# Performance work log

Measured on AMD Instinct MI355X. Metric: run time of the kernel, lower is better.

The kernel has to match this reference:

```python
import jax, jax.numpy as jnp
import numpy as np

B, S, V, E, H = 4096, 64, 100000, 128, 128

_PARAM_NAMES = ["Wz", "Uzl", "Uzr", "Wr", "Url", "Urr", "Wh", "Uhl", "Uhr"]


def setup_inputs() -> dict:
    key = jax.random.key(0)
    ks = jax.random.split(key, 2 + 2 * len(_PARAM_NAMES))
    inp = {"tokens": jax.random.randint(ks[0], (B, S), 0, V)}
    inp["emb"] = jax.random.normal(ks[1], (V, E), jnp.float32)
    i = 2
    for n in _PARAM_NAMES:
        din = E if n.startswith("W") else H
        inp[n] = jax.random.normal(ks[i], (din, H), jnp.float32) / np.sqrt(din).astype(np.float32)
        i += 1
        inp["b" + n] = jax.random.normal(ks[i], (H,), jnp.float32) * 0.01
        i += 1
    return inp


def _tree_gru(word, hl, hr, p):
    # word: [..., E], hl/hr: [..., H]
    z = jax.nn.sigmoid(word @ p["Wz"] + p["bWz"] + hl @ p["Uzl"] + p["bUzl"] + hr @ p["Uzr"] + p["bUzr"])
    r = jax.nn.sigmoid(word @ p["Wr"] + p["bWr"] + hl @ p["Url"] + p["bUrl"] + hr @ p["Urr"] + p["bUrr"])
    h_tilde = jnp.tanh(word @ p["Wh"] + p["bWh"] + (r * hl) @ p["Uhl"] + p["bUhl"] + (r * hr) @ p["Uhr"] + p["bUhr"])
    return z * hl + z * hr + (1.0 - z) * h_tilde


def reference(tokens, emb, Wz, bWz, Uzl, bUzl, Uzr, bUzr, Wr, bWr, Url, bUrl, Urr, bUrr, Wh, bWh, Uhl, bUhl, Uhr, bUhr):
    p = dict(Wz=Wz, bWz=bWz, Uzl=Uzl, bUzl=bUzl, Uzr=Uzr, bUzr=bUzr,
             Wr=Wr, bWr=bWr, Url=Url, bUrl=bUrl, Urr=Urr, bUrr=bUrr,
             Wh=Wh, bWh=bWh, Uhl=Uhl, bUhl=bUhl, Uhr=Uhr, bUhr=bUhr)
    x = emb[tokens]                                   # [B, S, E]
    h0 = jnp.zeros(x.shape[:2] + (H,), x.dtype)
    cur = _tree_gru(x, h0, h0, p)                     # leaf nodes [B, S, H]
    n = cur.shape[1]
    while n > 1:                                      # static loop over log2(S) tree levels
        left, right = cur[:, 0::2], cur[:, 1::2]      # pair adjacent nodes
        word0 = jnp.zeros(left.shape[:2] + (E,), cur.dtype)
        cur = _tree_gru(word0, left, right, p)
        n //= 2
    return cur.transpose(1, 0, 2)                     # [1, B, H] (matches torch transpose(0,1))
```

## Files before the change

kernel.cpp:

```cpp
#include <hip/hip_runtime.h>


typedef _Float16 half_t;
typedef __attribute__((ext_vector_type(8))) _Float16 f16x8;
typedef __attribute__((ext_vector_type(4))) float f32x4;

#define NTOK 262144
#define NB 4096
#define NV 100000

__device__ __forceinline__ float sigm(float x){
  float e = __expf(-x);
  return __builtin_amdgcn_rcpf(1.0f + e);
}
__device__ __forceinline__ float tanh_(float x){
  float xc = fminf(fmaxf(x,-15.f),15.f);
  float e = __expf(2.f*xc);
  return (e - 1.f) * __builtin_amdgcn_rcpf(e + 1.f);
}

__global__ void bias_k(const float* bWz,const float* bUzl,const float* bUzr,
                       const float* bWr,const float* bUrl,const float* bUrr,
                       const float* bWh,const float* bUhl,const float* bUhr, float* bc){
  int j = threadIdx.x;
  if (j < 128)      bc[j] = bWz[j]+bUzl[j]+bUzr[j];
  else if (j < 256){ int i=j-128; bc[j] = bWr[i]+bUrl[i]+bUrr[i]; }
  else if (j < 384){ int i=j-256; bc[j] = bWh[i]+bUhl[i]+bUhr[i]; }
}

__global__ __launch_bounds__(256) void wprep_k(
    const float* Wz, const float* Wh,
    const float* Uzl,const float* Uzr,const float* Url,const float* Urr,
    const float* Uhl,const float* Uhr, half_t* wb){
  int idx = blockIdx.x*256 + threadIdx.x;
  if (idx < 32768){
    const float* W = (idx < 16384) ? Wz : Wh;
    int t = idx & 16383;
    int w = t >> 11, ks = (t >> 9) & 3, l = (t >> 3) & 63, j = t & 7;
    int n = w*16 + (l & 15);
    int k = ks*32 + ((l >> 4) << 3) + j;
    wb[idx] = (half_t)W[k*128 + n];
  } else {
    int t = idx - 32768;
    int mat = t >> 15;
    t &= 32767;
    int w = t >> 12, ks = (t >> 9) & 7, l = (t >> 3) & 63, j = t & 7;
    int n = w*16 + (l & 15);
    int kp = ks*32 + ((l >> 4) << 3) + j;
    int k = kp >> 1;
    const float* U;
    if (mat == 0) U = (kp & 1) ? Uzr : Uzl;
    else if (mat == 1) U = (kp & 1) ? Urr : Url;
    else U = (kp & 1) ? Uhr : Uhl;
    wb[idx] = (half_t)U[k*128 + n];
  }
}

template<int MT>
__global__ __launch_bounds__(512, 4) void h1tab_k(
    const float* __restrict__ emb,
    const half_t* __restrict__ Wz_f, const half_t* __restrict__ Wh_f,
    const float* __restrict__ bc, half_t* __restrict__ t1)
{
  __shared__ __align__(16) _Float16 xs[MT*16][136];
  const int tid = threadIdx.x;
  const int m0  = blockIdx.x*(MT*16);
  #pragma unroll
  for (int it = 0; it < MT; it++){
    int idx = it*512 + tid;
    int m = idx >> 5, c = idx & 31;
    int row = m0 + m; if (row >= NV) row = 0;
    float4 v = ((const float4*)(emb + (size_t)row*128))[c];
    union { half_t h[4]; ushort4 u; } p;
    p.h[0]=(half_t)v.x; p.h[1]=(half_t)v.y; p.h[2]=(half_t)v.z; p.h[3]=(half_t)v.w;
    *(ushort4*)&xs[m][c*4] = p.u;
  }
  __syncthreads();
  const int w = tid>>6, l = tid&63;
  const int lr = l&15, lk = (l>>4)*8, lq = (l>>4)*4;
  const int col = w*16 + lr;

  f32x4 zacc[MT] = {}; f32x4 hacc[MT] = {};
  const half_t* wzp = Wz_f + ((w*4)*64 + l)*8;
  const half_t* whp = Wh_f + ((w*4)*64 + l)*8;
  f16x8 bz_n = *(const f16x8*)wzp;
  f16x8 bh_n = *(const f16x8*)whp;
  #pragma unroll
  for (int ks=0; ks<4; ks++){
    f16x8 bz = bz_n, bh = bh_n;
    if (ks < 3){
      bz_n = *(const f16x8*)(wzp + (ks+1)*512);
      bh_n = *(const f16x8*)(whp + (ks+1)*512);
    }
    #pragma unroll
    for (int mt=0; mt<MT; mt++){
      f16x8 a = *(const f16x8*)&xs[mt*16 + lr][ks*32 + lk];
      zacc[mt] = __builtin_amdgcn_mfma_f32_16x16x32_f16(a, bz, zacc[mt],0,0,0);
      hacc[mt] = __builtin_amdgcn_mfma_f32_16x16x32_f16(a, bh, hacc[mt],0,0,0);
    }
  }
  const float bzv = bc[col], bhv = bc[256+col];
  #pragma unroll
  for (int mt=0; mt<MT; mt++){
    #pragma unroll
    for (int q=0; q<4; q++){
      int row = m0 + mt*16 + lq + q;
      if (row < NV){
        float z  = sigm(zacc[mt][q] + bzv);
        float ht = tanh_(hacc[mt][q] + bhv);
        t1[(size_t)row*128 + col] = (half_t)((1.f-z)*ht);
      }
    }
  }
}

template<int MT, int GATHER>
__global__ __launch_bounds__(512, 4) void tree_k(
    const half_t* __restrict__ hin, const int* __restrict__ tokens,
    half_t* __restrict__ hout, float* __restrict__ outf,
    const half_t* __restrict__ Uz_f, const half_t* __restrict__ Ur_f, const half_t* __restrict__ Uh_f,
    const float* __restrict__ bc, int last)
{
  __shared__ __align__(16) _Float16 xs[MT*16][264];
  const int tid = threadIdx.x;
  const int m0  = blockIdx.x*(MT*16);
  #pragma unroll
  for (int it = 0; it < MT; it++){
    int idx = it*512 + tid;
    int m = idx >> 5, c = idx & 31;
    const half_t *pl, *pr;
    if (GATHER){
      int tl = tokens[2*(m0+m)], tr = tokens[2*(m0+m)+1];
      pl = hin + (size_t)tl*128 + c*4;
      pr = hin + (size_t)tr*128 + c*4;
    } else {
      size_t base = (size_t)(2*(m0+m))*128 + c*4;
      pl = hin + base;
      pr = hin + base + 128;
    }
    uint2 A  = *(const uint2*)pl;
    uint2 Bv = *(const uint2*)pr;
    uint4 o;
    o.x = (A.x & 0xFFFFu) | (Bv.x << 16);
    o.y = (A.x >> 16)     | (Bv.x & 0xFFFF0000u);
    o.z = (A.y & 0xFFFFu) | (Bv.y << 16);
    o.w = (A.y >> 16)     | (Bv.y & 0xFFFF0000u);
    *(uint4*)&xs[m][c*8] = o;
  }
  __syncthreads();
  const int w = tid>>6, l = tid&63;
  const int lr = l&15, lk = (l>>4)*8, lq = (l>>4)*4;
  const int col = w*16 + lr;

  f32x4 zacc[MT] = {}; f32x4 racc[MT] = {};
  const half_t* uzp = Uz_f + ((w*8)*64 + l)*8;
  const half_t* urp = Ur_f + ((w*8)*64 + l)*8;
  f16x8 bz_n = *(const f16x8*)uzp;
  f16x8 br_n = *(const f16x8*)urp;
  #pragma unroll
  for (int ks=0; ks<8; ks++){
    f16x8 bz = bz_n, br = br_n;
    if (ks < 7){
      bz_n = *(const f16x8*)(uzp + (ks+1)*512);
      br_n = *(const f16x8*)(urp + (ks+1)*512);
    }
    #pragma unroll
    for (int mt=0; mt<MT; mt++){
      f16x8 a = *(const f16x8*)&xs[mt*16 + lr][ks*32 + lk];
      zacc[mt] = __builtin_amdgcn_mfma_f32_16x16x32_f16(a, bz, zacc[mt],0,0,0);
      racc[mt] = __builtin_amdgcn_mfma_f32_16x16x32_f16(a, br, racc[mt],0,0,0);
    }
  }
  __syncthreads();

  uint zp[MT][2], sp[MT][2];
  const float bzv = bc[col], brv = bc[128+col];
  #pragma unroll
  for (int mt=0; mt<MT; mt++){
    union { half_t h[4]; uint u[2]; } pz, ps;
    #pragma unroll
    for (int q=0; q<4; q++){
      int row = mt*16 + lq + q;
      union { uint u; half_t h[2]; } io;
      io.u = *(uint*)&xs[row][2*col];
      float hl = (float)io.h[0];
      float hr = (float)io.h[1];
      float z  = sigm(zacc[mt][q] + bzv);
      float rv = sigm(racc[mt][q] + brv);
      pz.h[q] = (half_t)z;
      ps.h[q] = (half_t)(hl + hr);
      io.h[0] = (half_t)(rv*hl);
      io.h[1] = (half_t)(rv*hr);
      *(uint*)&xs[row][2*col] = io.u;
    }
    zp[mt][0]=pz.u[0]; zp[mt][1]=pz.u[1];
    sp[mt][0]=ps.u[0]; sp[mt][1]=ps.u[1];
  }
  __syncthreads();

  f32x4 ha[MT] = {};
  const half_t* uhp = Uh_f + ((w*8)*64 + l)*8;
  f16x8 bh_n = *(const f16x8*)uhp;
  #pragma unroll
  for (int ks=0; ks<8; ks++){
    f16x8 bh = bh_n;
    if (ks < 7) bh_n = *(const f16x8*)(uhp + (ks+1)*512);
    #pragma unroll
    for (int mt=0; mt<MT; mt++){
      f16x8 a = *(const f16x8*)&xs[mt*16 + lr][ks*32 + lk];
      ha[mt] = __builtin_amdgcn_mfma_f32_16x16x32_f16(a, bh, ha[mt],0,0,0);
    }
  }
  const float bhv = bc[256+col];
  #pragma unroll
  for (int mt=0; mt<MT; mt++){
    union { half_t h[4]; uint u[2]; } pz, ps;
    pz.u[0]=zp[mt][0]; pz.u[1]=zp[mt][1];
    ps.u[0]=sp[mt][0]; ps.u[1]=sp[mt][1];
    #pragma unroll
    for (int q=0; q<4; q++){
      int row = mt*16 + lq + q;
      float ht = tanh_(ha[mt][q] + bhv);
      float z  = (float)pz.h[q];
      float o  = z*(float)ps.h[q] + (1.f-z)*ht;
      size_t off = (size_t)(m0+row)*128 + col;
      if (last) outf[off] = o;
      else      hout[off] = (half_t)o;
    }
  }
}

extern "C" void kernel_launch(void* const* d_in, const int* in_sizes, int n_in,
                              void* d_out, int out_size, void* d_ws, size_t ws_size,
                              hipStream_t stream) {
  const int*   tokens = (const int*)  d_in[0];
  const float* emb    = (const float*)d_in[1];
  const float* Wz  = (const float*)d_in[2];  const float* bWz  = (const float*)d_in[3];
  const float* Uzl = (const float*)d_in[4];  const float* bUzl = (const float*)d_in[5];
  const float* Uzr = (const float*)d_in[6];  const float* bUzr = (const float*)d_in[7];
  const float* Wr  = (const float*)d_in[8];  const float* bWr  = (const float*)d_in[9];
  const float* Url = (const float*)d_in[10]; const float* bUrl = (const float*)d_in[11];
  const float* Urr = (const float*)d_in[12]; const float* bUrr = (const float*)d_in[13];
  const float* Wh  = (const float*)d_in[14]; const float* bWh  = (const float*)d_in[15];
  const float* Uhl = (const float*)d_in[16]; const float* bUhl = (const float*)d_in[17];
  const float* Uhr = (const float*)d_in[18]; const float* bUhr = (const float*)d_in[19];

  float*  bc = (float*)d_ws;
  half_t* wb = (half_t*)((char*)d_ws + 4096);
  half_t* Wz_f = wb;
  half_t* Wh_f = wb + 16384;
  half_t* Uz_f = wb + 32768;
  half_t* Ur_f = wb + 65536;
  half_t* Uh_f = wb + 98304;
  half_t* t1 = (half_t*)((char*)d_ws + (1<<20));
  half_t* hA = t1 + (size_t)NV*128;
  half_t* hB = hA + (size_t)(NTOK/2)*128;

  bias_k<<<1, 384, 0, stream>>>(bWz,bUzl,bUzr,bWr,bUrl,bUrr,bWh,bUhl,bUhr, bc);
  wprep_k<<<512, 256, 0, stream>>>(Wz,Wh,Uzl,Uzr,Url,Urr,Uhl,Uhr, wb);

  h1tab_k<8><<<(NV + 127)/128, 512, 0, stream>>>(emb, Wz_f, Wh_f, bc, t1);

  tree_k<8,1><<<(NTOK/2)/128, 512, 0, stream>>>(t1, tokens, hA, (float*)d_out,
                                                Uz_f, Ur_f, Uh_f, bc, 0);
  const half_t* src = hA;
  half_t* other = hB;
  for (int lvl = 2; lvl <= 6; lvl++){
    int M = NB << (6 - lvl);
    int last = (lvl == 6);
    half_t* dst = other;
    if (M >= 32768){
      tree_k<8,0><<<M/128, 512, 0, stream>>>(src, tokens, dst, (float*)d_out,
                                             Uz_f, Ur_f, Uh_f, bc, last);
    } else if (M >= 16384){
      tree_k<4,0><<<M/64, 512, 0, stream>>>(src, tokens, dst, (float*)d_out,
                                            Uz_f, Ur_f, Uh_f, bc, last);
    } else {
      tree_k<2,0><<<M/32, 512, 0, stream>>>(src, tokens, dst, (float*)d_out,
                                            Uz_f, Ur_f, Uh_f, bc, last);
    }
    other = (half_t*)src;
    src = dst;
  }
}
```

Measured before the change: 149.8 us.

## Switch tree GRU kernel to 32x32x16 MFMA with row-group wave tiling

Replaces the 16x16x32 MFMA tiles in the tree kernel with 32x32x16 MFMA, reorganising waves into column groups and row groups, and re-packs the U weight fragments to match. Launch shapes per level are rewritten: larger row tiles for early levels and smaller blocks for the final levels. The intent is to cut per-wave instruction and LDS-read overhead and to reuse each weight fragment across more rows. In exchange the accumulators grow (16 floats per tile), which raises register pressure, and the deepest levels run only 128 blocks.

```diff
diff --git a/kernel.cpp b/kernel.cpp
--- a/kernel.cpp
+++ b/kernel.cpp
@@ -4,6 +4,7 @@
 typedef _Float16 half_t;
 typedef __attribute__((ext_vector_type(8))) _Float16 f16x8;
 typedef __attribute__((ext_vector_type(4))) float f32x4;
+typedef __attribute__((ext_vector_type(16))) float f32x16;
 
 #define NTOK 262144
 #define NB 4096
@@ -44,9 +45,9 @@
     int t = idx - 32768;
     int mat = t >> 15;
     t &= 32767;
-    int w = t >> 12, ks = (t >> 9) & 7, l = (t >> 3) & 63, j = t & 7;
-    int n = w*16 + (l & 15);
-    int kp = ks*32 + ((l >> 4) << 3) + j;
+    int cg = t >> 13, ks = (t >> 9) & 15, l = (t >> 3) & 63, j = t & 7;
+    int n = cg*32 + (l & 31);
+    int kp = ks*16 + ((l >> 5) << 3) + j;
     int k = kp >> 1;
     const float* U;
     if (mat == 0) U = (kp & 1) ? Uzr : Uzl;
@@ -114,19 +115,21 @@
   }
 }
 
-template<int MT, int GATHER>
-__global__ __launch_bounds__(512, 4) void tree_k(
+template<int MT, int WR, int GATHER>
+__global__ __launch_bounds__(WR*256, 4) void tree_k(
     const half_t* __restrict__ hin, const int* __restrict__ tokens,
     half_t* __restrict__ hout, float* __restrict__ outf,
     const half_t* __restrict__ Uz_f, const half_t* __restrict__ Ur_f, const half_t* __restrict__ Uh_f,
     const float* __restrict__ bc, int last)
 {
-  __shared__ __align__(16) _Float16 xs[MT*16][264];
+  constexpr int ROWS = WR*MT*32;
+  constexpr int THREADS = WR*256;
+  __shared__ __align__(16) _Float16 xs[ROWS][264];
   const int tid = threadIdx.x;
-  const int m0  = blockIdx.x*(MT*16);
-  #pragma unroll
-  for (int it = 0; it < MT; it++){
-    int idx = it*512 + tid;
+  const int m0  = blockIdx.x*ROWS;
+  #pragma unroll
+  for (int it = 0; it < MT*4; it++){
+    int idx = it*THREADS + tid;
     int m = idx >> 5, c = idx & 31;
     const half_t *pl, *pr;
     if (GATHER){
@@ -149,80 +152,83 @@
   }
   __syncthreads();
   const int w = tid>>6, l = tid&63;
-  const int lr = l&15, lk = (l>>4)*8, lq = (l>>4)*4;
-  const int col = w*16 + lr;
-
-  f32x4 zacc[MT] = {}; f32x4 racc[MT] = {};
-  const half_t* uzp = Uz_f + ((w*8)*64 + l)*8;
-  const half_t* urp = Ur_f + ((w*8)*64 + l)*8;
+  const int cg = w & 3, rg = w >> 2;
+  const int lc = l & 31, hi = l >> 5;
+  const int lk8 = hi*8;
+  const int col = cg*32 + lc;
+  const int rowbase = rg*(MT*32);
+
+  f32x16 zacc[MT] = {}; f32x16 racc[MT] = {};
+  const half_t* uzp = Uz_f + ((cg*16)*64 + l)*8;
+  const half_t* urp = Ur_f + ((cg*16)*64 + l)*8;
   f16x8 bz_n = *(const f16x8*)uzp;
   f16x8 br_n = *(const f16x8*)urp;
   #pragma unroll
-  for (int ks=0; ks<8; ks++){
+  for (int ks=0; ks<16; ks++){
     f16x8 bz = bz_n, br = br_n;
-    if (ks < 7){
+    if (ks < 15){
       bz_n = *(const f16x8*)(uzp + (ks+1)*512);
       br_n = *(const f16x8*)(urp + (ks+1)*512);
     }
     #pragma unroll
     for (int mt=0; mt<MT; mt++){
-      f16x8 a = *(const f16x8*)&xs[mt*16 + lr][ks*32 + lk];
-      zacc[mt] = __builtin_amdgcn_mfma_f32_16x16x32_f16(a, bz, zacc[mt],0,0,0);
-      racc[mt] = __builtin_amdgcn_mfma_f32_16x16x32_f16(a, br, racc[mt],0,0,0);
-    }
-  }
-  __syncthreads();
-
-  uint zp[MT][2], sp[MT][2];
+      f16x8 a = *(const f16x8*)&xs[rowbase + mt*32 + lc][ks*16 + lk8];
+      zacc[mt] = __builtin_amdgcn_mfma_f32_32x32x16_f16(a, bz, zacc[mt],0,0,0);
+      racc[mt] = __builtin_amdgcn_mfma_f32_32x32x16_f16(a, br, racc[mt],0,0,0);
+    }
+  }
+  __syncthreads();
+
+  uint zp[MT][8], sp[MT][8];
   const float bzv = bc[col], brv = bc[128+col];
   #pragma unroll
   for (int mt=0; mt<MT; mt++){
-    union { half_t h[4]; uint u[2]; } pz, ps;
-    #pragma unroll
-    for (int q=0; q<4; q++){
-      int row = mt*16 + lq + q;
+    union { half_t h[16]; uint u[8]; } pz, ps;
+    #pragma unroll
+    for (int r=0; r<16; r++){
+      int row = rowbase + mt*32 + (r&3) + 8*(r>>2) + 4*hi;
       union { uint u; half_t h[2]; } io;
       io.u = *(uint*)&xs[row][2*col];
       float hl = (float)io.h[0];
       float hr = (float)io.h[1];
-      float z  = sigm(zacc[mt][q] + bzv);
-      float rv = sigm(racc[mt][q] + brv);
-      pz.h[q] = (half_t)z;
-      ps.h[q] = (half_t)(hl + hr);
+      float z  = sigm(zacc[mt][r] + bzv);
+      float rv = sigm(racc[mt][r] + brv);
+      pz.h[r] = (half_t)z;
+      ps.h[r] = (half_t)(hl + hr);
       io.h[0] = (half_t)(rv*hl);
       io.h[1] = (half_t)(rv*hr);
       *(uint*)&xs[row][2*col] = io.u;
     }
-    zp[mt][0]=pz.u[0]; zp[mt][1]=pz.u[1];
-    sp[mt][0]=ps.u[0]; sp[mt][1]=ps.u[1];
-  }
-  __syncthreads();
-
-  f32x4 ha[MT] = {};
-  const half_t* uhp = Uh_f + ((w*8)*64 + l)*8;
+    #pragma unroll
+    for (int u8=0; u8<8; u8++){ zp[mt][u8]=pz.u[u8]; sp[mt][u8]=ps.u[u8]; }
+  }
+  __syncthreads();
+
+  f32x16 ha[MT] = {};
+  const half_t* uhp = Uh_f + ((cg*16)*64 + l)*8;
   f16x8 bh_n = *(const f16x8*)uhp;
   #pragma unroll
-  for (int ks=0; ks<8; ks++){
+  for (int ks=0; ks<16; ks++){
     f16x8 bh = bh_n;
-    if (ks < 7) bh_n = *(const f16x8*)(uhp + (ks+1)*512);
+    if (ks < 15) bh_n = *(const f16x8*)(uhp + (ks+1)*512);
     #pragma unroll
     for (int mt=0; mt<MT; mt++){
-      f16x8 a = *(const f16x8*)&xs[mt*16 + lr][ks*32 + lk];
-      ha[mt] = __builtin_amdgcn_mfma_f32_16x16x32_f16(a, bh, ha[mt],0,0,0);
+      f16x8 a = *(const f16x8*)&xs[rowbase + mt*32 + lc][ks*16 + lk8];
+      ha[mt] = __builtin_amdgcn_mfma_f32_32x32x16_f16(a, bh, ha[mt],0,0,0);
     }
   }
   const float bhv = bc[256+col];
   #pragma unroll
   for (int mt=0; mt<MT; mt++){
-    union { half_t h[4]; uint u[2]; } pz, ps;
-    pz.u[0]=zp[mt][0]; pz.u[1]=zp[mt][1];
-    ps.u[0]=sp[mt][0]; ps.u[1]=sp[mt][1];
-    #pragma unroll
-    for (int q=0; q<4; q++){
-      int row = mt*16 + lq + q;
-      float ht = tanh_(ha[mt][q] + bhv);
-      float z  = (float)pz.h[q];
-      float o  = z*(float)ps.h[q] + (1.f-z)*ht;
+    union { half_t h[16]; uint u[8]; } pz, ps;
+    #pragma unroll
+    for (int u8=0; u8<8; u8++){ pz.u[u8]=zp[mt][u8]; ps.u[u8]=sp[mt][u8]; }
+    #pragma unroll
+    for (int r=0; r<16; r++){
+      int row = rowbase + mt*32 + (r&3) + 8*(r>>2) + 4*hi;
+      float ht = tanh_(ha[mt][r] + bhv);
+      float z  = (float)pz.h[r];
+      float o  = z*(float)ps.h[r] + (1.f-z)*ht;
       size_t off = (size_t)(m0+row)*128 + col;
       if (last) outf[off] = o;
       else      hout[off] = (half_t)o;
@@ -261,25 +267,11 @@
 
   h1tab_k<8><<<(NV + 127)/128, 512, 0, stream>>>(emb, Wz_f, Wh_f, bc, t1);
 
-  tree_k<8,1><<<(NTOK/2)/128, 512, 0, stream>>>(t1, tokens, hA, (float*)d_out,
-                                                Uz_f, Ur_f, Uh_f, bc, 0);
-  const half_t* src = hA;
-  half_t* other = hB;
-  for (int lvl = 2; lvl <= 6; lvl++){
-    int M = NB << (6 - lvl);
-    int last = (lvl == 6);
-    half_t* dst = other;
-    if (M >= 32768){
-      tree_k<8,0><<<M/128, 512, 0, stream>>>(src, tokens, dst, (float*)d_out,
-                                             Uz_f, Ur_f, Uh_f, bc, last);
-    } else if (M >= 16384){
-      tree_k<4,0><<<M/64, 512, 0, stream>>>(src, tokens, dst, (float*)d_out,
-                                            Uz_f, Ur_f, Uh_f, bc, last);
-    } else {
-      tree_k<2,0><<<M/32, 512, 0, stream>>>(src, tokens, dst, (float*)d_out,
-                                            Uz_f, Ur_f, Uh_f, bc, last);
-    }
-    other = (half_t*)src;
-    src = dst;
-  }
-}
+  float* outf = (float*)d_out;
+  tree_k<2,2,1><<<1024, 512, 0, stream>>>(t1, tokens, hA, outf, Uz_f, Ur_f, Uh_f, bc, 0);
+  tree_k<2,2,0><<<512, 512, 0, stream>>>(hA, tokens, hB, outf, Uz_f, Ur_f, Uh_f, bc, 0);
+  tree_k<2,2,0><<<256, 512, 0, stream>>>(hB, tokens, hA, outf, Uz_f, Ur_f, Uh_f, bc, 0);
+  tree_k<2,2,0><<<128, 512, 0, stream>>>(hA, tokens, hB, outf, Uz_f, Ur_f, Uh_f, bc, 0);
+  tree_k<1,2,0><<<128, 512, 0, stream>>>(hB, tokens, hA, outf, Uz_f, Ur_f, Uh_f, bc, 0);
+  tree_k<1,1,0><<<128, 256, 0, stream>>>(hA, tokens, hB, outf, Uz_f, Ur_f, Uh_f, bc, 1);
+}
```

Result: slower. 156.7 us (+4.6%).

## Fuse tree levels two through six into one shared-memory kernel

Applied to the files above, without the earlier changes.

Replaces the five per-level tree kernel launches with a single tail kernel. Each block loads 128 level-1 nodes and runs the remaining levels in LDS, passing intermediate states between two shared buffers, so the intermediate global writes and reads are gone. Bias folding moves into the weight-prep kernel, the tanh formulation is simplified, and h1tab uses smaller tiles with higher occupancy. The cost is that later levels run on small, partly empty tiles, with extra syncs and idle MFMA work.

```diff
diff --git a/kernel.cpp b/kernel.cpp
--- a/kernel.cpp
+++ b/kernel.cpp
@@ -2,6 +2,7 @@
 
 
 typedef _Float16 half_t;
+typedef __attribute__((ext_vector_type(2))) _Float16 f16x2;
 typedef __attribute__((ext_vector_type(8))) _Float16 f16x8;
 typedef __attribute__((ext_vector_type(4))) float f32x4;
 
@@ -14,24 +15,19 @@
   return __builtin_amdgcn_rcpf(1.0f + e);
 }
 __device__ __forceinline__ float tanh_(float x){
-  float xc = fminf(fmaxf(x,-15.f),15.f);
-  float e = __expf(2.f*xc);
-  return (e - 1.f) * __builtin_amdgcn_rcpf(e + 1.f);
-}
-
-__global__ void bias_k(const float* bWz,const float* bUzl,const float* bUzr,
-                       const float* bWr,const float* bUrl,const float* bUrr,
-                       const float* bWh,const float* bUhl,const float* bUhr, float* bc){
-  int j = threadIdx.x;
-  if (j < 128)      bc[j] = bWz[j]+bUzl[j]+bUzr[j];
-  else if (j < 256){ int i=j-128; bc[j] = bWr[i]+bUrl[i]+bUrr[i]; }
-  else if (j < 384){ int i=j-256; bc[j] = bWh[i]+bUhl[i]+bUhr[i]; }
+  float e = __expf(2.f*x);
+  float r = __builtin_amdgcn_rcpf(1.0f + e);
+  return __builtin_fmaf(-2.0f, r, 1.0f);
 }
 
 __global__ __launch_bounds__(256) void wprep_k(
     const float* Wz, const float* Wh,
     const float* Uzl,const float* Uzr,const float* Url,const float* Urr,
-    const float* Uhl,const float* Uhr, half_t* wb){
+    const float* Uhl,const float* Uhr,
+    const float* bWz,const float* bUzl,const float* bUzr,
+    const float* bWr,const float* bUrl,const float* bUrr,
+    const float* bWh,const float* bUhl,const float* bUhr,
+    half_t* wb, float* bc){
   int idx = blockIdx.x*256 + threadIdx.x;
   if (idx < 32768){
     const float* W = (idx < 16384) ? Wz : Wh;
@@ -54,10 +50,16 @@
     else U = (kp & 1) ? Uhr : Uhl;
     wb[idx] = (half_t)U[k*128 + n];
   }
+  if (blockIdx.x == 511 && threadIdx.x < 128){
+    int j = threadIdx.x;
+    bc[j]       = bWz[j] + bUzl[j] + bUzr[j];
+    bc[128 + j] = bWr[j] + bUrl[j] + bUrr[j];
+    bc[256 + j] = bWh[j] + bUhl[j] + bUhr[j];
+  }
 }
 
 template<int MT>
-__global__ __launch_bounds__(512, 4) void h1tab_k(
+__global__ __launch_bounds__(512, 8) void h1tab_k(
     const float* __restrict__ emb,
     const half_t* __restrict__ Wz_f, const half_t* __restrict__ Wh_f,
     const float* __restrict__ bc, half_t* __restrict__ t1)
@@ -83,15 +85,10 @@
   f32x4 zacc[MT] = {}; f32x4 hacc[MT] = {};
   const half_t* wzp = Wz_f + ((w*4)*64 + l)*8;
   const half_t* whp = Wh_f + ((w*4)*64 + l)*8;
-  f16x8 bz_n = *(const f16x8*)wzp;
-  f16x8 bh_n = *(const f16x8*)whp;
   #pragma unroll
   for (int ks=0; ks<4; ks++){
-    f16x8 bz = bz_n, bh = bh_n;
-    if (ks < 3){
-      bz_n = *(const f16x8*)(wzp + (ks+1)*512);
-      bh_n = *(const f16x8*)(whp + (ks+1)*512);
-    }
+    f16x8 bz = *(const f16x8*)(wzp + ks*512);
+    f16x8 bh = *(const f16x8*)(whp + ks*512);
     #pragma unroll
     for (int mt=0; mt<MT; mt++){
       f16x8 a = *(const f16x8*)&xs[mt*16 + lr][ks*32 + lk];
@@ -114,12 +111,12 @@
   }
 }
 
-template<int MT, int GATHER>
-__global__ __launch_bounds__(512, 4) void tree_k(
+template<int MT>
+__global__ __launch_bounds__(512, 4) void tree1_k(
     const half_t* __restrict__ hin, const int* __restrict__ tokens,
-    half_t* __restrict__ hout, float* __restrict__ outf,
+    half_t* __restrict__ hout,
     const half_t* __restrict__ Uz_f, const half_t* __restrict__ Ur_f, const half_t* __restrict__ Uh_f,
-    const float* __restrict__ bc, int last)
+    const float* __restrict__ bc)
 {
   __shared__ __align__(16) _Float16 xs[MT*16][264];
   const int tid = threadIdx.x;
@@ -128,18 +125,9 @@
   for (int it = 0; it < MT; it++){
     int idx = it*512 + tid;
     int m = idx >> 5, c = idx & 31;
-    const half_t *pl, *pr;
-    if (GATHER){
-      int tl = tokens[2*(m0+m)], tr = tokens[2*(m0+m)+1];
-      pl = hin + (size_t)tl*128 + c*4;
-      pr = hin + (size_t)tr*128 + c*4;
-    } else {
-      size_t base = (size_t)(2*(m0+m))*128 + c*4;
-      pl = hin + base;
-      pr = hin + base + 128;
-    }
-    uint2 A  = *(const uint2*)pl;
-    uint2 Bv = *(const uint2*)pr;
+    int tl = tokens[2*(m0+m)], tr = tokens[2*(m0+m)+1];
+    uint2 A  = *(const uint2*)(hin + (size_t)tl*128 + c*4);
+    uint2 Bv = *(const uint2*)(hin + (size_t)tr*128 + c*4);
     uint4 o;
     o.x = (A.x & 0xFFFFu) | (Bv.x << 16);
     o.y = (A.x >> 16)     | (Bv.x & 0xFFFF0000u);
@@ -152,7 +140,7 @@
   const int lr = l&15, lk = (l>>4)*8, lq = (l>>4)*4;
   const int col = w*16 + lr;
 
-  f32x4 zacc[MT] = {}; f32x4 racc[MT] = {};
+  f32x4 zacc[MT] = {}, racc[MT] = {};
   const half_t* uzp = Uz_f + ((w*8)*64 + l)*8;
   const half_t* urp = Ur_f + ((w*8)*64 + l)*8;
   f16x8 bz_n = *(const f16x8*)uzp;
@@ -223,11 +211,124 @@
       float ht = tanh_(ha[mt][q] + bhv);
       float z  = (float)pz.h[q];
       float o  = z*(float)ps.h[q] + (1.f-z)*ht;
-      size_t off = (size_t)(m0+row)*128 + col;
-      if (last) outf[off] = o;
-      else      hout[off] = (half_t)o;
-    }
-  }
+      hout[(size_t)(m0+row)*128 + col] = (half_t)o;
+    }
+  }
+}
+
+template<int MT, int RV, int LAST>
+static __device__ __forceinline__ void level_step(
+    _Float16 (*X)[264], _Float16 (*Y)[264], int tid,
+    const half_t* Uz_f, const half_t* Ur_f, const half_t* Uh_f,
+    const float* bc, float* outf, int outrow0)
+{
+  const int w = tid>>6, l = tid&63;
+  const int lr = l&15, lk = (l>>4)*8, lq = (l>>4)*4;
+  const int col = w*16 + lr;
+
+  f32x4 zacc[MT] = {}, racc[MT] = {};
+  const half_t* uzp = Uz_f + ((w*8)*64 + l)*8;
+  const half_t* urp = Ur_f + ((w*8)*64 + l)*8;
+  #pragma unroll
+  for (int ks=0; ks<8; ks++){
+    f16x8 bz = *(const f16x8*)(uzp + ks*512);
+    f16x8 br = *(const f16x8*)(urp + ks*512);
+    #pragma unroll
+    for (int mt=0; mt<MT; mt++){
+      f16x8 a = *(const f16x8*)&X[mt*16 + lr][ks*32 + lk];
+      zacc[mt] = __builtin_amdgcn_mfma_f32_16x16x32_f16(a, bz, zacc[mt],0,0,0);
+      racc[mt] = __builtin_amdgcn_mfma_f32_16x16x32_f16(a, br, racc[mt],0,0,0);
+    }
+  }
+  __syncthreads();
+
+  uint zp[MT][2], sp[MT][2];
+  const float bzv = bc[col], brv = bc[128+col];
+  #pragma unroll
+  for (int mt=0; mt<MT; mt++){
+    union { half_t h[4]; uint u[2]; } pz, ps;
+    #pragma unroll
+    for (int q=0; q<4; q++){
+      int row = mt*16 + lq + q;
+      union { uint u; half_t h[2]; } io;
+      io.u = *(uint*)&X[row][2*col];
+      float hl = (float)io.h[0];
+      float hr = (float)io.h[1];
+      float z  = sigm(zacc[mt][q] + bzv);
+      float rv = sigm(racc[mt][q] + brv);
+      pz.h[q] = (half_t)z;
+      ps.h[q] = (half_t)(hl + hr);
+      io.h[0] = (half_t)(rv*hl);
+      io.h[1] = (half_t)(rv*hr);
+      *(uint*)&X[row][2*col] = io.u;
+    }
+    zp[mt][0]=pz.u[0]; zp[mt][1]=pz.u[1];
+    sp[mt][0]=ps.u[0]; sp[mt][1]=ps.u[1];
+  }
+  __syncthreads();
+
+  f32x4 ha[MT] = {};
+  const half_t* uhp = Uh_f + ((w*8)*64 + l)*8;
+  #pragma unroll
+  for (int ks=0; ks<8; ks++){
+    f16x8 bh = *(const f16x8*)(uhp + ks*512);
+    #pragma unroll
+    for (int mt=0; mt<MT; mt++){
+      f16x8 a = *(const f16x8*)&X[mt*16 + lr][ks*32 + lk];
+      ha[mt] = __builtin_amdgcn_mfma_f32_16x16x32_f16(a, bh, ha[mt],0,0,0);
+    }
+  }
+  const float bhv = bc[256+col];
+  #pragma unroll
+  for (int mt=0; mt<MT; mt++){
+    union { half_t h[4]; uint u[2]; } pz, ps;
+    pz.u[0]=zp[mt][0]; pz.u[1]=zp[mt][1];
+    ps.u[0]=sp[mt][0]; ps.u[1]=sp[mt][1];
+    #pragma unroll
+    for (int q=0; q<4; q++){
+      int row = mt*16 + lq + q;
+      if (row < RV){
+        float ht = tanh_(ha[mt][q] + bhv);
+        float z  = (float)pz.h[q];
+        float o  = z*(float)ps.h[q] + (1.f-z)*ht;
+        if (LAST) outf[(size_t)(outrow0 + row)*128 + col] = o;
+        else      Y[row>>1][2*col + (row&1)] = (half_t)o;
+      }
+    }
+  }
+  __syncthreads();
+}
+
+__global__ __launch_bounds__(512, 6) void tree_tail_k(
+    const half_t* __restrict__ hA, float* __restrict__ outf,
+    const half_t* __restrict__ Uz_f, const half_t* __restrict__ Ur_f, const half_t* __restrict__ Uh_f,
+    const float* __restrict__ bc)
+{
+  __shared__ __align__(16) _Float16 XA[64][264];
+  __shared__ __align__(16) _Float16 XB[32][264];
+  const int tid = threadIdx.x;
+  const int g = blockIdx.x;
+  #pragma unroll
+  for (int it = 0; it < 4; it++){
+    int idx = it*512 + tid;
+    int m = idx >> 5, c = idx & 31;
+    int b = m >> 4, i = m & 15;
+    size_t base = ((size_t)(128*g + b*32 + 2*i))*128 + c*4;
+    uint2 A  = *(const uint2*)(hA + base);
+    uint2 Bv = *(const uint2*)(hA + base + 128);
+    uint4 o;
+    o.x = (A.x & 0xFFFFu) | (Bv.x << 16);
+    o.y = (A.x >> 16)     | (Bv.x & 0xFFFF0000u);
+    o.z = (A.y & 0xFFFFu) | (Bv.y << 16);
+    o.w = (A.y >> 16)     | (Bv.y & 0xFFFF0000u);
+    *(uint4*)&XA[m][c*8] = o;
+  }
+  __syncthreads();
+  level_step<4,64,0>(XA, XB, tid, Uz_f, Ur_f, Uh_f, bc, outf, 0);
+  level_step<2,32,0>(XB, XA, tid, Uz_f, Ur_f, Uh_f, bc, outf, 0);
+  level_step<1,16,0>(XA, XB, tid, Uz_f, Ur_f, Uh_f, bc, outf, 0);
+  level_step<1, 8,0>(XB, XA, tid, Uz_f, Ur_f, Uh_f, bc, outf, 0);
+  level_step<1, 4,1>(XA, XB, tid, Uz_f, Ur_f, Uh_f, bc, outf, 4*g);
 }
 
 extern "C" void kernel_launch(void* const* d_in, const int* in_sizes, int n_in,
@@ -254,32 +355,13 @@
   half_t* Uh_f = wb + 98304;
   half_t* t1 = (half_t*)((char*)d_ws + (1<<20));
   half_t* hA = t1 + (size_t)NV*128;
-  half_t* hB = hA + (size_t)(NTOK/2)*128;
-
-  bias_k<<<1, 384, 0, stream>>>(bWz,bUzl,bUzr,bWr,bUrl,bUrr,bWh,bUhl,bUhr, bc);
-  wprep_k<<<512, 256, 0, stream>>>(Wz,Wh,Uzl,Uzr,Url,Urr,Uhl,Uhr, wb);
-
-  h1tab_k<8><<<(NV + 127)/128, 512, 0, stream>>>(emb, Wz_f, Wh_f, bc, t1);
-
-  tree_k<8,1><<<(NTOK/2)/128, 512, 0, stream>>>(t1, tokens, hA, (float*)d_out,
-                                                Uz_f, Ur_f, Uh_f, bc, 0);
-  const half_t* src = hA;
-  half_t* other = hB;
-  for (int lvl = 2; lvl <= 6; lvl++){
-    int M = NB << (6 - lvl);
-    int last = (lvl == 6);
-    half_t* dst = other;
-    if (M >= 32768){
-      tree_k<8,0><<<M/128, 512, 0, stream>>>(src, tokens, dst, (float*)d_out,
-                                             Uz_f, Ur_f, Uh_f, bc, last);
-    } else if (M >= 16384){
-      tree_k<4,0><<<M/64, 512, 0, stream>>>(src, tokens, dst, (float*)d_out,
-                                            Uz_f, Ur_f, Uh_f, bc, last);
-    } else {
-      tree_k<2,0><<<M/32, 512, 0, stream>>>(src, tokens, dst, (float*)d_out,
-                                            Uz_f, Ur_f, Uh_f, bc, last);
-    }
-    other = (half_t*)src;
-    src = dst;
-  }
-}
+
+  wprep_k<<<512, 256, 0, stream>>>(Wz,Wh,Uzl,Uzr,Url,Urr,Uhl,Uhr,
+                                   bWz,bUzl,bUzr,bWr,bUrl,bUrr,bWh,bUhl,bUhr, wb, bc);
+
+  h1tab_k<4><<<(NV + 63)/64, 512, 0, stream>>>(emb, Wz_f, Wh_f, bc, t1);
+
+  tree1_k<8><<<(NTOK/2)/128, 512, 0, stream>>>(t1, tokens, hA, Uz_f, Ur_f, Uh_f, bc);
+
+  tree_tail_k<<<1024, 512, 0, stream>>>(hA, (float*)d_out, Uz_f, Ur_f, Uh_f, bc);
+}
```

Result: faster. 135.8 us (-9.4%).
